# Optimization experiments

Measured on AMD Instinct MI355X. Metric: run time of the kernel, lower is better.

## Reference

```python
import math
import jax, jax.numpy as jnp
import numpy as np

B, NQ, NKV, D, H = 32, 512, 512, 1024, 8
DH = D // H              # 128
N_COLS = 512             # n + 1
D_COL = math.ceil(2 * math.log2(N_COLS))  # 18


def setup_inputs() -> dict:
    key = jax.random.key(0)
    ks = jax.random.split(key, 8)
    s = 0.02
    return {
        "x_q": jax.random.normal(ks[0], (B, NQ, D), jnp.float32),
        "x_kv": jax.random.normal(ks[1], (B, NKV, D), jnp.float32),
        # sym_weight=True => W_tail is W_head (shared)
        "W_head_w": jax.random.normal(ks[2], (D, D), jnp.float32) * s,
        "W_head_b": jnp.zeros((D,), jnp.float32),
        "W_v_w": jax.random.normal(ks[3], (D, D), jnp.float32) * s,
        "W_v_b": jnp.zeros((D,), jnp.float32),
        "W_out_w": jax.random.normal(ks[4], (D, D), jnp.float32) * s,
        "W_out_b": jnp.zeros((D,), jnp.float32),
        "rel_emb": jnp.ones((H, DH), jnp.float32),
        "col_head": jax.random.normal(ks[5], (H, N_COLS, D_COL), jnp.float32) * 0.2,
        "col_tail": jax.random.normal(ks[6], (H, N_COLS, D_COL), jnp.float32) * 0.2,
    }


def _heads(x, W, b, h, dh):
    # Linear then split heads: [B, n, d] -> [B, H, n, dh]
    B_, n, _ = x.shape
    y = x @ W.T + b
    return y.reshape(B_, n, h, dh).transpose(0, 2, 1, 3)


def reference(x_q, x_kv, W_head_w, W_head_b, W_v_w, W_v_b,
              W_out_w, W_out_b, rel_emb, col_head, col_tail):
    Bb, nq, d = x_q.shape
    nkv = x_kv.shape[1]
    h, dh = rel_emb.shape

    f_head = _heads(x_q, W_head_w, W_head_b, h, dh) * rel_emb[None, :, None, :]
    f_tail = _heads(x_kv, W_head_w, W_head_b, h, dh) * rel_emb[None, :, None, :]  # W_tail = W_head (sym_weight)
    f_v = _heads(x_kv, W_v_w, W_v_b, h, dh)

    # content score: [B, H, nq, nkv]
    weight_score = jnp.einsum('bhqd,bhkd->bhqk', f_head, f_tail) / math.sqrt(dh)

    # learned column topology: [H, n_cols, n_cols]
    adj_logits = jnp.einsum('hqc,hkc->hqk', col_head, col_tail)
    eye = jnp.eye(adj_logits.shape[-1], dtype=bool)  # nsi: zero diagonal before softmax
    adj_logits = jnp.where(eye[None], 0.0, adj_logits)
    adj = jax.nn.softmax(adj_logits, axis=-1)[:, :nq, :nkv]

    adj_mask = (1.0 - adj) * -10000.0
    fr_graph = jax.nn.softmax(weight_score + adj_mask[None], axis=-1)

    x = jnp.einsum('bhqk,bhkd->bhqd', fr_graph, f_v)
    x = x.transpose(0, 2, 1, 3).reshape(Bb, nq, h * dh)
    x = x @ W_out_w.T + W_out_b
    return (x, fr_graph.reshape(Bb * h, nq, nkv))
```

## Files before the change

### kernel.cpp

```cpp
#include <hip/hip_runtime.h>

typedef __attribute__((ext_vector_type(8))) __bf16 bf8;
typedef __attribute__((ext_vector_type(4))) __bf16 bf4;
typedef __attribute__((ext_vector_type(4))) float f32x4;

#define DEVI static __device__ __forceinline__

DEVI void gload_lds16(const void* g, void* l) {
  __builtin_amdgcn_global_load_lds(
      (const __attribute__((address_space(1))) unsigned int*)g,
      (__attribute__((address_space(3))) unsigned int*)l, 16, 0, 0);
}

__global__ __launch_bounds__(256) void cvt_kernel(const float* __restrict__ in,
                                                  __bf16* __restrict__ out, int n4) {
  int stride = gridDim.x * blockDim.x;
  for (int i = blockIdx.x * blockDim.x + threadIdx.x; i < n4; i += stride) {
    f32x4 v = reinterpret_cast<const f32x4*>(in)[i];
    bf4 o;
    o[0] = (__bf16)v[0]; o[1] = (__bf16)v[1]; o[2] = (__bf16)v[2]; o[3] = (__bf16)v[3];
    reinterpret_cast<bf4*>(out)[i] = o;
  }
}

template <int MODE>
__global__ __launch_bounds__(256) void gemm_proj(
    const __bf16* __restrict__ A, const __bf16* __restrict__ Bw,
    const float* __restrict__ bias, const float* __restrict__ rel,
    __bf16* __restrict__ obf, float* __restrict__ of32) {
  __shared__ alignas(16) __bf16 As[128 * 64];
  __shared__ alignas(16) __bf16 Bs[128 * 64];
  const int tid = threadIdx.x;
  const int lane = tid & 63;
  const int wave = tid >> 6;
  const int wr = wave >> 1, wc = wave & 1;
  const int lr = lane & 15, lk = (lane >> 4) * 8;
  const int bm = blockIdx.x, bn = blockIdx.y;

  f32x4 acc[4][4];
#pragma unroll
  for (int i = 0; i < 4; ++i)
#pragma unroll
    for (int j = 0; j < 4; ++j)
#pragma unroll
      for (int e = 0; e < 4; ++e) acc[i][j][e] = 0.f;

  const __bf16* Ab = A + (size_t)bm * 128 * 1024;
  const __bf16* Bb = Bw + (size_t)bn * 128 * 1024;
  const int sr = tid >> 3;
  const int sc = (tid & 7) * 8;

  for (int kt = 0; kt < 1024; kt += 64) {
#pragma unroll
    for (int i = 0; i < 4; ++i) {
      gload_lds16(Ab + (size_t)(sr + i * 32) * 1024 + kt + sc, As + tid * 8 + i * 2048);
      gload_lds16(Bb + (size_t)(sr + i * 32) * 1024 + kt + sc, Bs + tid * 8 + i * 2048);
    }
    __syncthreads();
#pragma unroll
    for (int kk = 0; kk < 64; kk += 32) {
      bf8 a[4], b[4];
#pragma unroll
      for (int mi = 0; mi < 4; ++mi)
        a[mi] = *reinterpret_cast<const bf8*>(&As[(wr * 64 + mi * 16 + lr) * 64 + kk + lk]);
#pragma unroll
      for (int ni = 0; ni < 4; ++ni)
        b[ni] = *reinterpret_cast<const bf8*>(&Bs[(wc * 64 + ni * 16 + lr) * 64 + kk + lk]);
#pragma unroll
      for (int mi = 0; mi < 4; ++mi)
#pragma unroll
        for (int ni = 0; ni < 4; ++ni)
          acc[mi][ni] = __builtin_amdgcn_mfma_f32_16x16x32_bf16(a[mi], b[ni], acc[mi][ni], 0, 0, 0);
    }
    __syncthreads();
  }

  const int mBase = bm * 128 + wr * 64;
  const int nBase = bn * 128 + wc * 64;
#pragma unroll
  for (int mi = 0; mi < 4; ++mi) {
#pragma unroll
    for (int ni = 0; ni < 4; ++ni) {
      const int n = nBase + ni * 16 + lr;
#pragma unroll
      for (int r = 0; r < 4; ++r) {
        const int m = mBase + mi * 16 + (lane >> 4) * 4 + r;
        float v = acc[mi][ni][r] + bias[n];
        if (MODE == 0) v *= rel[n];
        if (MODE == 2) {
          of32[(size_t)m * 1024 + n] = v;
        } else if (MODE == 0) {
          size_t idx = ((size_t)((m >> 9) * 8 + (n >> 7))) * 65536 +
                       (size_t)(m & 511) * 128 + (n & 127);
          obf[idx] = (__bf16)v;
        } else {
          size_t idx = ((size_t)((m >> 9) * 8 + (n >> 7))) * 65536 +
                       (size_t)(n & 127) * 512 + (m & 511);
          obf[idx] = (__bf16)v;
        }
      }
    }
  }
}

__global__ __launch_bounds__(256) void adj_kernel(const float* __restrict__ ch_all,
                                                  const float* __restrict__ ct_all,
                                                  __bf16* __restrict__ adjT) {
  const int wave = threadIdx.x >> 6, lane = threadIdx.x & 63;
  const int row = blockIdx.x * 4 + wave;
  const int h = row >> 9, i = row & 511;
  float ch[18];
  const float* chp = ch_all + ((size_t)h * 512 + i) * 18;
#pragma unroll
  for (int t = 0; t < 18; ++t) ch[t] = chp[t];
  float e[8];
  float m = -1e30f;
#pragma unroll
  for (int jj = 0; jj < 8; ++jj) {
    const int j = jj * 64 + lane;
    const float* ctp = ct_all + ((size_t)h * 512 + j) * 18;
    float d = 0.f;
#pragma unroll
    for (int t = 0; t < 18; ++t) d += ch[t] * ctp[t];
    if (j == i) d = 0.f;
    e[jj] = d;
    m = fmaxf(m, d);
  }
#pragma unroll
  for (int off = 32; off >= 1; off >>= 1) m = fmaxf(m, __shfl_xor(m, off));
  float s = 0.f;
#pragma unroll
  for (int jj = 0; jj < 8; ++jj) { e[jj] = __expf(e[jj] - m); s += e[jj]; }
#pragma unroll
  for (int off = 32; off >= 1; off >>= 1) s += __shfl_xor(s, off);
  const float inv = 10000.f / s;
  __bf16* op = adjT + (size_t)h * 262144 + i;
#pragma unroll
  for (int jj = 0; jj < 8; ++jj)
    op[(size_t)(jj * 64 + lane) * 512] = (__bf16)(e[jj] * inv - 19.53125f);
}

__global__ __launch_bounds__(256, 3) void fused_attn_kernel(
    const __bf16* __restrict__ fh, const __bf16* __restrict__ ft,
    const __bf16* __restrict__ fvT, const __bf16* __restrict__ adjT,
    float* __restrict__ fr, __bf16* __restrict__ ctx) {
  __shared__ alignas(16) __bf16 Bt[128 * 128];
  __shared__ alignas(16) __bf16 Pl[4][16 * 128];
  const int tid = threadIdx.x;
  const int l = tid & 63, w = tid >> 6;
  const int b = blockIdx.x;
  const int h = blockIdx.y >> 3;
  const int qt = blockIdx.y & 7;
  const int bh = b * 8 + h;
  const int wrow = qt * 64 + w * 16;
  const int lr = l & 15;
  const int khi = l >> 4;

  const int srow = tid >> 4;
  const int scc = (tid & 15) ^ (srow & 7);

  bf8 afr[4];
  {
    const __bf16* ap = fh + (size_t)bh * 65536 + (size_t)(wrow + lr) * 128 + khi * 8;
#pragma unroll
    for (int kk4 = 0; kk4 < 4; ++kk4)
      afr[kk4] = *reinterpret_cast<const bf8*>(ap + kk4 * 32);
  }

  f32x4 acc[32];
#pragma unroll
  for (int n = 0; n < 32; ++n)
#pragma unroll
    for (int e = 0; e < 4; ++e) acc[n][e] = 0.f;

  const __bf16* ftb = ft + (size_t)bh * 65536;
#pragma unroll
  for (int kt = 0; kt < 4; ++kt) {
#pragma unroll
    for (int i = 0; i < 8; ++i)
      gload_lds16(ftb + (size_t)(kt * 128 + i * 16 + srow) * 128 + scc * 8,
                  Bt + i * 2048 + tid * 8);
    __syncthreads();
    __builtin_amdgcn_s_setprio(1);
#pragma unroll
    for (int kk4 = 0; kk4 < 4; ++kk4) {
      bf8 bfr[8];
#pragma unroll
      for (int n2 = 0; n2 < 8; ++n2)
        bfr[n2] = *reinterpret_cast<const bf8*>(
            &Bt[(n2 * 16 + lr) * 128 + ((kk4 * 4 + khi) ^ (lr & 7)) * 8]);
#pragma unroll
      for (int n2 = 0; n2 < 8; ++n2)
        acc[kt * 8 + n2] =
            __builtin_amdgcn_mfma_f32_16x16x32_bf16(afr[kk4], bfr[n2], acc[kt * 8 + n2], 0, 0, 0);
    }
    __builtin_amdgcn_s_setprio(0);
    __syncthreads();
  }

  const float scale = 0.08838834764831845f;
  const __bf16* adjTp = adjT + (size_t)h * 262144;
  float mrow[4] = {-1e30f, -1e30f, -1e30f, -1e30f};
#pragma unroll
  for (int n = 0; n < 32; ++n) {
    const int col = n * 16 + lr;
    bf4 av4 = *reinterpret_cast<const bf4*>(adjTp + (size_t)col * 512 + wrow + khi * 4);
#pragma unroll
    for (int r = 0; r < 4; ++r) {
      float v = acc[n][r] * scale + (float)av4[r];
      acc[n][r] = v;
      mrow[r] = fmaxf(mrow[r], v);
    }
  }
#pragma unroll
  for (int r = 0; r < 4; ++r)
#pragma unroll
    for (int off = 1; off <= 8; off <<= 1) mrow[r] = fmaxf(mrow[r], __shfl_xor(mrow[r], off));
  float srw[4] = {0.f, 0.f, 0.f, 0.f};
#pragma unroll
  for (int n = 0; n < 32; ++n)
#pragma unroll
    for (int r = 0; r < 4; ++r) {
      float e = __expf(acc[n][r] - mrow[r]);
      acc[n][r] = e;
      srw[r] += e;
    }
#pragma unroll
  for (int r = 0; r < 4; ++r)
#pragma unroll
    for (int off = 1; off <= 8; off <<= 1) srw[r] += __shfl_xor(srw[r], off);
  float inv[4];
#pragma unroll
  for (int r = 0; r < 4; ++r) inv[r] = 1.f / srw[r];
#pragma unroll
  for (int n = 0; n < 32; ++n)
#pragma unroll
    for (int r = 0; r < 4; ++r) acc[n][r] *= inv[r];

  const __bf16* fvb = fvT + (size_t)bh * 65536;
#pragma unroll
  for (int i = 0; i < 8; ++i)
    gload_lds16(fvb + (size_t)(i * 16 + srow) * 512 + scc * 8, Bt + i * 2048 + tid * 8);

  {
    float* frb = fr + (size_t)bh * 262144;
#pragma unroll
    for (int n = 0; n < 32; ++n) {
      const int col = n * 16 + lr;
#pragma unroll
      for (int r = 0; r < 4; ++r)
        frb[(size_t)(wrow + khi * 4 + r) * 512 + col] = acc[n][r];
    }
  }

  f32x4 acc2[8];
#pragma unroll
  for (int n2 = 0; n2 < 8; ++n2)
#pragma unroll
    for (int e = 0; e < 4; ++e) acc2[n2][e] = 0.f;

  __bf16* Pw = &Pl[w][0];
#pragma unroll
  for (int kt = 0; kt < 4; ++kt) {
#pragma unroll
    for (int n2 = 0; n2 < 8; ++n2) {
      const int colc = n2 * 2 + (lr >> 3);
      const int cl = lr & 7;
#pragma unroll
      for (int r = 0; r < 4; ++r) {
        const int q = khi * 4 + r;
        Pw[q * 128 + ((colc ^ (q & 7)) * 8) + cl] = (__bf16)acc[kt * 8 + n2][r];
      }
    }
    __syncthreads();
    __builtin_amdgcn_s_setprio(1);
#pragma unroll
    for (int kk4 = 0; kk4 < 4; ++kk4) {
      bf8 pa = *reinterpret_cast<const bf8*>(
          &Pw[lr * 128 + ((kk4 * 4 + khi) ^ (lr & 7)) * 8]);
      bf8 bfr[8];
#pragma unroll
      for (int n2 = 0; n2 < 8; ++n2)
        bfr[n2] = *reinterpret_cast<const bf8*>(
            &Bt[(n2 * 16 + lr) * 128 + ((kk4 * 4 + khi) ^ (lr & 7)) * 8]);
#pragma unroll
      for (int n2 = 0; n2 < 8; ++n2)
        acc2[n2] = __builtin_amdgcn_mfma_f32_16x16x32_bf16(pa, bfr[n2], acc2[n2], 0, 0, 0);
    }
    __builtin_amdgcn_s_setprio(0);
    __syncthreads();
    if (kt < 3) {
      const int ktn = kt + 1;
#pragma unroll
      for (int i = 0; i < 8; ++i)
        gload_lds16(fvb + (size_t)(i * 16 + srow) * 512 + ktn * 128 + scc * 8,
                    Bt + i * 2048 + tid * 8);
    }
  }

#pragma unroll
  for (int n2 = 0; n2 < 8; ++n2) {
    const int c = n2 * 16 + lr;
#pragma unroll
    for (int r = 0; r < 4; ++r) {
      const int q = wrow + khi * 4 + r;
      ctx[(size_t)(b * 512 + q) * 1024 + h * 128 + c] = (__bf16)acc2[n2][r];
    }
  }
}

extern "C" void kernel_launch(void* const* d_in, const int* in_sizes, int n_in,
                              void* d_out, int out_size, void* d_ws, size_t ws_size,
                              hipStream_t stream) {
  const float* x_q  = (const float*)d_in[0];
  const float* x_kv = (const float*)d_in[1];
  const float* Wh   = (const float*)d_in[2];
  const float* bh   = (const float*)d_in[3];
  const float* Wv   = (const float*)d_in[4];
  const float* bv   = (const float*)d_in[5];
  const float* Wo   = (const float*)d_in[6];
  const float* bo   = (const float*)d_in[7];
  const float* rel  = (const float*)d_in[8];
  const float* colh = (const float*)d_in[9];
  const float* colt = (const float*)d_in[10];

  float* out = (float*)d_out;
  float* fr  = out + 16777216;

  __bf16* xq_bf  = (__bf16*)d_ws;
  __bf16* xkv_bf = xq_bf + 16777216;
  __bf16* Wh_bf  = xkv_bf + 16777216;
  __bf16* Wv_bf  = Wh_bf + 1048576;
  __bf16* Wo_bf  = Wv_bf + 1048576;
  __bf16* fhead  = Wo_bf + 1048576;
  __bf16* ftail  = fhead + 16777216;
  __bf16* fvT    = ftail + 16777216;
  __bf16* adjT   = fvT + 16777216;
  __bf16* ctx    = adjT + 2097152;

  cvt_kernel<<<4096, 256, 0, stream>>>(x_q, xq_bf, 4194304);
  cvt_kernel<<<4096, 256, 0, stream>>>(x_kv, xkv_bf, 4194304);
  cvt_kernel<<<1024, 256, 0, stream>>>(Wh, Wh_bf, 262144);
  cvt_kernel<<<1024, 256, 0, stream>>>(Wv, Wv_bf, 262144);
  cvt_kernel<<<1024, 256, 0, stream>>>(Wo, Wo_bf, 262144);

  dim3 gp(128, 8);
  gemm_proj<0><<<gp, 256, 0, stream>>>(xq_bf, Wh_bf, bh, rel, fhead, nullptr);
  gemm_proj<0><<<gp, 256, 0, stream>>>(xkv_bf, Wh_bf, bh, rel, ftail, nullptr);
  gemm_proj<1><<<gp, 256, 0, stream>>>(xkv_bf, Wv_bf, bv, nullptr, fvT, nullptr);

  adj_kernel<<<1024, 256, 0, stream>>>(colh, colt, adjT);

  fused_attn_kernel<<<dim3(32, 64), 256, 0, stream>>>(fhead, ftail, fvT, adjT, fr, ctx);

  gemm_proj<2><<<gp, 256, 0, stream>>>(ctx, Wo_bf, bo, nullptr, nullptr, out);
}
```

Measured before the change: 878.1 us.

## Double-buffer projection GEMM with 256x256 tiles and swizzled LDS

Reworks the projection GEMM to use 256x256 output tiles with 512 threads, double-buffered LDS staging with explicit vmcnt waits and barriers, and an XOR swizzle on LDS columns to cut bank conflicts. Global loads for the next K tile now overlap MFMA work on the current one, and each block reuses its loaded data over a larger tile. The cost is 128KB of LDS per block and higher register pressure from 32 accumulators per wave, which may restrict occupancy. The grid also shrinks to 256 blocks, which could leave some CUs underused.

```diff
diff --git a/kernel.cpp b/kernel.cpp
--- a/kernel.cpp
+++ b/kernel.cpp
@@ -11,6 +11,14 @@
       (const __attribute__((address_space(1))) unsigned int*)g,
       (__attribute__((address_space(3))) unsigned int*)l, 16, 0, 0);
 }
+
+#define WAITV(N)                                             \
+  asm volatile("s_waitcnt vmcnt(" #N ")" ::: "memory");      \
+  __builtin_amdgcn_sched_barrier(0)
+#define BARRIER()                      \
+  __builtin_amdgcn_sched_barrier(0);   \
+  __builtin_amdgcn_s_barrier();        \
+  __builtin_amdgcn_sched_barrier(0)
 
 __global__ __launch_bounds__(256) void cvt_kernel(const float* __restrict__ in,
                                                   __bf16* __restrict__ out, int n4) {
@@ -24,67 +32,95 @@
 }
 
 template <int MODE>
-__global__ __launch_bounds__(256) void gemm_proj(
+__global__ __launch_bounds__(512, 2) void gemm_proj(
     const __bf16* __restrict__ A, const __bf16* __restrict__ Bw,
     const float* __restrict__ bias, const float* __restrict__ rel,
     __bf16* __restrict__ obf, float* __restrict__ of32) {
-  __shared__ alignas(16) __bf16 As[128 * 64];
-  __shared__ alignas(16) __bf16 Bs[128 * 64];
+  __shared__ alignas(16) __bf16 As0[256 * 64];
+  __shared__ alignas(16) __bf16 Bs0[256 * 64];
+  __shared__ alignas(16) __bf16 As1[256 * 64];
+  __shared__ alignas(16) __bf16 Bs1[256 * 64];
   const int tid = threadIdx.x;
   const int lane = tid & 63;
   const int wave = tid >> 6;
-  const int wr = wave >> 1, wc = wave & 1;
-  const int lr = lane & 15, lk = (lane >> 4) * 8;
+  const int wr = wave >> 2;
+  const int wc = wave & 3;
+  const int lr = lane & 15;
+  const int khi = lane >> 4;
   const int bm = blockIdx.x, bn = blockIdx.y;
 
-  f32x4 acc[4][4];
-#pragma unroll
-  for (int i = 0; i < 4; ++i)
-#pragma unroll
-    for (int j = 0; j < 4; ++j)
-#pragma unroll
-      for (int e = 0; e < 4; ++e) acc[i][j][e] = 0.f;
-
-  const __bf16* Ab = A + (size_t)bm * 128 * 1024;
-  const __bf16* Bb = Bw + (size_t)bn * 128 * 1024;
-  const int sr = tid >> 3;
-  const int sc = (tid & 7) * 8;
-
-  for (int kt = 0; kt < 1024; kt += 64) {
-#pragma unroll
-    for (int i = 0; i < 4; ++i) {
-      gload_lds16(Ab + (size_t)(sr + i * 32) * 1024 + kt + sc, As + tid * 8 + i * 2048);
-      gload_lds16(Bb + (size_t)(sr + i * 32) * 1024 + kt + sc, Bs + tid * 8 + i * 2048);
-    }
-    __syncthreads();
-#pragma unroll
-    for (int kk = 0; kk < 64; kk += 32) {
-      bf8 a[4], b[4];
-#pragma unroll
-      for (int mi = 0; mi < 4; ++mi)
-        a[mi] = *reinterpret_cast<const bf8*>(&As[(wr * 64 + mi * 16 + lr) * 64 + kk + lk]);
+  const __bf16* Ab = A + (size_t)bm * 256 * 1024;
+  const __bf16* Bb = Bw + (size_t)bn * 256 * 1024;
+
+  const int srow = tid >> 3;
+  const int scc = (tid & 7) ^ (srow & 7);
+
+  f32x4 acc[8][4];
+#pragma unroll
+  for (int mi = 0; mi < 8; ++mi)
+#pragma unroll
+    for (int ni = 0; ni < 4; ++ni)
+#pragma unroll
+      for (int e = 0; e < 4; ++e) acc[mi][ni][e] = 0.f;
+
+  auto STAGE = [&](const __bf16* gb, __bf16* lds, int kt) {
+#pragma unroll
+    for (int i = 0; i < 4; ++i)
+      gload_lds16(gb + (size_t)(i * 64 + srow) * 1024 + kt * 64 + scc * 8,
+                  lds + i * 4096 + tid * 8);
+  };
+
+  auto COMPUTE = [&](const __bf16* As, const __bf16* Bs) {
+    __builtin_amdgcn_s_setprio(1);
+#pragma unroll
+    for (int kk = 0; kk < 2; ++kk) {
+      const int ck = ((kk * 4 + khi) ^ (lr & 7)) * 8;
+      bf8 a[8], b[4];
+#pragma unroll
+      for (int mi = 0; mi < 8; ++mi)
+        a[mi] = *reinterpret_cast<const bf8*>(&As[(wr * 128 + mi * 16 + lr) * 64 + ck]);
 #pragma unroll
       for (int ni = 0; ni < 4; ++ni)
-        b[ni] = *reinterpret_cast<const bf8*>(&Bs[(wc * 64 + ni * 16 + lr) * 64 + kk + lk]);
-#pragma unroll
-      for (int mi = 0; mi < 4; ++mi)
+        b[ni] = *reinterpret_cast<const bf8*>(&Bs[(wc * 64 + ni * 16 + lr) * 64 + ck]);
+#pragma unroll
+      for (int mi = 0; mi < 8; ++mi)
 #pragma unroll
         for (int ni = 0; ni < 4; ++ni)
           acc[mi][ni] = __builtin_amdgcn_mfma_f32_16x16x32_bf16(a[mi], b[ni], acc[mi][ni], 0, 0, 0);
     }
-    __syncthreads();
-  }
-
-  const int mBase = bm * 128 + wr * 64;
-  const int nBase = bn * 128 + wc * 64;
-#pragma unroll
-  for (int mi = 0; mi < 4; ++mi) {
+    __builtin_amdgcn_s_setprio(0);
+  };
+
+  STAGE(Ab, As0, 0); STAGE(Bb, Bs0, 0);
+  STAGE(Ab, As1, 1); STAGE(Bb, Bs1, 1);
+
+  for (int it = 0; it < 7; ++it) {
+    WAITV(8);
+    BARRIER();
+    COMPUTE(As0, Bs0);
+    BARRIER();
+    STAGE(Ab, As0, 2 * it + 2); STAGE(Bb, Bs0, 2 * it + 2);
+    WAITV(8);
+    BARRIER();
+    COMPUTE(As1, Bs1);
+    BARRIER();
+    STAGE(Ab, As1, 2 * it + 3); STAGE(Bb, Bs1, 2 * it + 3);
+  }
+  WAITV(8);
+  BARRIER();
+  COMPUTE(As0, Bs0);
+  WAITV(0);
+  BARRIER();
+  COMPUTE(As1, Bs1);
+
+#pragma unroll
+  for (int mi = 0; mi < 8; ++mi) {
 #pragma unroll
     for (int ni = 0; ni < 4; ++ni) {
-      const int n = nBase + ni * 16 + lr;
+      const int n = bn * 256 + wc * 64 + ni * 16 + lr;
 #pragma unroll
       for (int r = 0; r < 4; ++r) {
-        const int m = mBase + mi * 16 + (lane >> 4) * 4 + r;
+        const int m = bm * 256 + wr * 128 + mi * 16 + khi * 4 + r;
         float v = acc[mi][ni][r] + bias[n];
         if (MODE == 0) v *= rel[n];
         if (MODE == 2) {
@@ -344,14 +380,14 @@
   cvt_kernel<<<1024, 256, 0, stream>>>(Wv, Wv_bf, 262144);
   cvt_kernel<<<1024, 256, 0, stream>>>(Wo, Wo_bf, 262144);
 
-  dim3 gp(128, 8);
-  gemm_proj<0><<<gp, 256, 0, stream>>>(xq_bf, Wh_bf, bh, rel, fhead, nullptr);
-  gemm_proj<0><<<gp, 256, 0, stream>>>(xkv_bf, Wh_bf, bh, rel, ftail, nullptr);
-  gemm_proj<1><<<gp, 256, 0, stream>>>(xkv_bf, Wv_bf, bv, nullptr, fvT, nullptr);
+  dim3 gp(64, 4);
+  gemm_proj<0><<<gp, 512, 0, stream>>>(xq_bf, Wh_bf, bh, rel, fhead, nullptr);
+  gemm_proj<0><<<gp, 512, 0, stream>>>(xkv_bf, Wh_bf, bh, rel, ftail, nullptr);
+  gemm_proj<1><<<gp, 512, 0, stream>>>(xkv_bf, Wv_bf, bv, nullptr, fvT, nullptr);
 
   adj_kernel<<<1024, 256, 0, stream>>>(colh, colt, adjT);
 
   fused_attn_kernel<<<dim3(32, 64), 256, 0, stream>>>(fhead, ftail, fvT, adjT, fr, ctx);
 
-  gemm_proj<2><<<gp, 256, 0, stream>>>(ctx, Wo_bf, bo, nullptr, nullptr, out);
-}
+  gemm_proj<2><<<gp, 512, 0, stream>>>(ctx, Wo_bf, bo, nullptr, nullptr, out);
+}
```

After: 817.1 us. 6.9% less time.
